# Performance work log

Hardware: AMD Instinct MI355X
Metric: run time of the kernel (lower is better)

The kernel has to match this reference:

```python
import jax, jax.numpy as jnp
import numpy as np

KERNEL_MUL = 2.0
KERNEL_NUM = 5


def setup_inputs() -> dict:
    key = jax.random.key(0)
    k1, k2 = jax.random.split(key)
    source = jax.random.normal(k1, (4096, 256), dtype=jnp.float32)
    target = jax.random.normal(k2, (4096, 256), dtype=jnp.float32)
    return {"source": source, "target": target}


def reference(source, target):
    n = source.shape[0]
    total = jnp.concatenate([source, target], axis=0)  # [2N, D]
    n_samples = total.shape[0]
    # Pairwise squared L2 distances via the norms trick (same math as
    # the broadcasted (total0 - total1)**2 sum, without the O(N^2 D) tensor).
    sq = jnp.sum(total * total, axis=-1)  # [2N]
    l2 = sq[:, None] + sq[None, :] - 2.0 * (total @ total.T)  # [2N, 2N]
    # Bandwidth is computed from .data in torch -> detached.
    bandwidth = jax.lax.stop_gradient(jnp.sum(l2)) / (n_samples ** 2 - n_samples)
    bandwidth = bandwidth / (KERNEL_MUL ** (KERNEL_NUM // 2))
    kernels = jnp.zeros_like(l2)
    for i in range(KERNEL_NUM):
        kernels = kernels + jnp.exp(-l2 / (bandwidth * KERNEL_MUL ** i))
    xx = kernels[:n, :n]
    yy = kernels[n:, n:]
    xy = kernels[:n, n:]
    yx = kernels[n:, :n]
    return jnp.mean(xx + yy - xy - yx)
```

## Files before the change

### kernel.cpp

```cpp
#include <hip/hip_runtime.h>
#include <hip/hip_bf16.h>
#if !__has_builtin(__builtin_amdgcn_cvt_pk_fp8_f32)
#include <hip/hip_fp8.h>
#endif

typedef unsigned char u8;
typedef unsigned short u16;
typedef long long i64;
typedef i64 i64x2 __attribute__((ext_vector_type(2)));
typedef float f32x4 __attribute__((ext_vector_type(4)));

#define NROW 8192
#define NHALF 4096
#define DIM 256
#define TILES 64
#define NBLK (TILES * (TILES + 1) / 2)
#define PBLK 512

static __device__ __forceinline__ float fast_exp2(float x) {
#if __has_builtin(__builtin_amdgcn_exp2f)
  return __builtin_amdgcn_exp2f(x);
#else
  return exp2f(x);
#endif
}

static __device__ __forceinline__ unsigned pack4_fp8(float4 v) {
#if __has_builtin(__builtin_amdgcn_cvt_pk_fp8_f32)
  int p = 0;
  p = __builtin_amdgcn_cvt_pk_fp8_f32(v.x, v.y, p, false);
  p = __builtin_amdgcn_cvt_pk_fp8_f32(v.z, v.w, p, true);
  return (unsigned)p;
#else
  __hip_fp8_e4m3 a(v.x), b(v.y), c(v.z), d(v.w);
  return (unsigned)a.__x | ((unsigned)b.__x << 8) | ((unsigned)c.__x << 16) |
         ((unsigned)d.__x << 24);
#endif
}


__global__ void k_prep(const float* __restrict__ src, const float* __restrict__ tgt,
                       u8* __restrict__ Xq, float* __restrict__ sq,
                       float* __restrict__ colpart) {
  __shared__ float cps[4][DIM];
  int w = threadIdx.x >> 6, lane = threadIdx.x & 63;
  int s = blockIdx.x;
  int r0 = s * 16 + w * 4;
  int p = lane >> 4, h = (lane >> 3) & 1, q = (lane >> 1) & 3, j = 4 * (lane & 1);
  float4 ca = make_float4(0.f, 0.f, 0.f, 0.f);
#pragma unroll
  for (int rr = 0; rr < 4; ++rr) {
    int row = r0 + rr;
    const float* pp = (row < NHALF) ? (src + (size_t)row * DIM)
                                    : (tgt + (size_t)(row - NHALF) * DIM);
    float4 v = *(const float4*)(pp + lane * 4);
    size_t di = ((size_t)(s * 4 + p) * 64 + q * 16 + (row & 15)) * 16 + h * 8 + j;
    *(unsigned*)(Xq + di) = pack4_fp8(v);
    ca.x += v.x; ca.y += v.y; ca.z += v.z; ca.w += v.w;
    float sum = v.x * v.x + v.y * v.y + v.z * v.z + v.w * v.w;
#pragma unroll
    for (int off = 32; off > 0; off >>= 1) sum += __shfl_down(sum, off);
    if (lane == 0) sq[row] = sum;
  }
  cps[w][lane * 4 + 0] = ca.x;
  cps[w][lane * 4 + 1] = ca.y;
  cps[w][lane * 4 + 2] = ca.z;
  cps[w][lane * 4 + 3] = ca.w;
  __syncthreads();
  int cc = threadIdx.x;
  colpart[blockIdx.x * DIM + cc] = cps[0][cc] + cps[1][cc] + cps[2][cc] + cps[3][cc];
}

__global__ void k_red(const float* __restrict__ colpart, float* __restrict__ colpart2) {
  int b = blockIdx.x, c = threadIdx.x;
  float s = 0.f;
#pragma unroll
  for (int i = 0; i < 16; ++i) s += colpart[(size_t)(b * 16 + i) * DIM + c];
  colpart2[b * DIM + c] = s;
}

__global__ void k_scal(const float* __restrict__ sq, const float* __restrict__ colpart2,
                       float* __restrict__ scal) {
  int c = threadIdx.x, lane = c & 63, w = c >> 6;
  float vs = 0.f;
#pragma unroll
  for (int b = 0; b < 32; ++b) vs += colpart2[b * DIM + c];
  float vn = vs * vs;
  float ss = 0.f;
#pragma unroll
  for (int k = 0; k < NROW / DIM; ++k) ss += sq[k * DIM + c];
#pragma unroll
  for (int off = 32; off > 0; off >>= 1) {
    vn += __shfl_down(vn, off);
    ss += __shfl_down(ss, off);
  }
  __shared__ float rv[4], rs[4];
  if (lane == 0) { rv[w] = vn; rs[w] = ss; }
  __syncthreads();
  if (c == 0) {
    double S  = (double)rs[0] + rs[1] + rs[2] + rs[3];
    double VN = (double)rv[0] + rv[1] + rv[2] + rv[3];
    double suml2 = 2.0 * (double)NROW * S - 2.0 * VN;
    double bw = suml2 / ((double)NROW * NROW - NROW) / 4.0;
    scal[0] = (float)(1.4426950408889634 / (bw * 16.0));
  }
  if (c < 32) scal[16 + c * 16] = 0.f;
}

__global__ __launch_bounds__(256, 4) void k_main(const u8* __restrict__ Xq,
                                                 const float* __restrict__ sq,
                                                 const float* __restrict__ scal,
                                                 float* __restrict__ accbuf) {
  __shared__ float red[4];

  int bi = 0, rem = blockIdx.x;
  while (rem >= TILES - bi) { rem -= TILES - bi; ++bi; }
  int bj = bi + rem;

  int tid = threadIdx.x;
  int w = tid >> 6, lane = tid & 63;
  int wi = w >> 1, wj = w & 1;

  f32x4 acc[4][4];
#pragma unroll
  for (int a = 0; a < 4; ++a)
#pragma unroll
    for (int b = 0; b < 4; ++b) acc[a][b] = (f32x4){0.f, 0.f, 0.f, 0.f};

  const i64x2* X2 = (const i64x2*)Xq;
  const int sA = bi * 8 + wi * 4;
  const int sB = bj * 8 + wj * 4;

#pragma unroll
  for (int p = 0; p < 4; ++p) {
    i64x2 aP[4], bP[4];
#pragma unroll
    for (int mi = 0; mi < 4; ++mi)
      aP[mi] = X2[(size_t)((sA + mi) * 4 + p) * 64 + lane];
#pragma unroll
    for (int ni = 0; ni < 4; ++ni)
      bP[ni] = X2[(size_t)((sB + ni) * 4 + p) * 64 + lane];
#pragma unroll
    for (int mi = 0; mi < 4; ++mi)
#pragma unroll
      for (int ni = 0; ni < 4; ++ni)
        acc[mi][ni] = __builtin_amdgcn_mfma_f32_16x16x32_fp8_fp8(
            aP[mi].x, bP[ni].x, acc[mi][ni], 0, 0, 0);
#pragma unroll
    for (int mi = 0; mi < 4; ++mi)
#pragma unroll
      for (int ni = 0; ni < 4; ++ni)
        acc[mi][ni] = __builtin_amdgcn_mfma_f32_16x16x32_fp8_fp8(
            aP[mi].y, bP[ni].y, acc[mi][ni], 0, 0, 0);
  }

  float c4 = scal[0];
  float wgt = ((bi < 32) == (bj < 32)) ? 1.f : -1.f;
  if (bi != bj) wgt *= 2.f;
  bool diag = (bi == bj);
  int ib = bi * 128 + wi * 64 + (lane >> 4) * 4;
  int jb = bj * 128 + wj * 64 + (lane & 15);
  f32x4 sqi[4];
#pragma unroll
  for (int mi = 0; mi < 4; ++mi) sqi[mi] = *(const f32x4*)(sq + ib + mi * 16);
  float lsum = 0.f;
#pragma unroll
  for (int ni = 0; ni < 4; ++ni) {
    float sqj = sq[jb + ni * 16];
#pragma unroll
    for (int mi = 0; mi < 4; ++mi) {
#pragma unroll
      for (int r = 0; r < 4; ++r) {
        float l2 = sqi[mi][r] + sqj - 2.f * acc[mi][ni][r];
        float t  = fast_exp2(-l2 * c4);
        float t2 = t * t, t4 = t2 * t2, t8 = t4 * t4, t16 = t8 * t8;
        float tt = t + t2 + t4 + t8 + t16;
        if (diag && (ib + mi * 16 + r) == (jb + ni * 16)) tt = 5.f;
        lsum += tt;
      }
    }
  }
#pragma unroll
  for (int off = 32; off > 0; off >>= 1) lsum += __shfl_down(lsum, off);
  if (lane == 0) red[w] = lsum;
  __syncthreads();
  if (tid == 0)
    atomicAdd(accbuf + (blockIdx.x & 31) * 16,
              wgt * (red[0] + red[1] + red[2] + red[3]));
}

__global__ void k_fin(const float* __restrict__ accbuf, float* __restrict__ out) {
  int lane = threadIdx.x & 63;
  float s = (lane < 32) ? accbuf[lane * 16] : 0.f;
#pragma unroll
  for (int off = 32; off > 0; off >>= 1) s += __shfl_down(s, off);
  if (threadIdx.x == 0) out[0] = s / 16777216.f;
}

extern "C" void kernel_launch(void* const* d_in, const int* in_sizes, int n_in,
                              void* d_out, int out_size, void* d_ws, size_t ws_size,
                              hipStream_t stream) {
  const float* src = (const float*)d_in[0];
  const float* tgt = (const float*)d_in[1];
  char* ws = (char*)d_ws;
  u8* Xq = (u8*)ws;
  size_t off = (size_t)NROW * DIM;
  float* sq = (float*)(ws + off);        off += NROW * 4;
  float* colpart = (float*)(ws + off);   off += (size_t)PBLK * DIM * 4;
  float* colpart2 = (float*)(ws + off);  off += (size_t)32 * DIM * 4;
  float* scal = (float*)(ws + off);
  float* out = (float*)d_out;

  k_prep<<<PBLK, 256, 0, stream>>>(src, tgt, Xq, sq, colpart);
  k_red<<<32, 256, 0, stream>>>(colpart, colpart2);
  k_scal<<<1, 256, 0, stream>>>(sq, colpart2, scal);
  k_main<<<NBLK, 256, 0, stream>>>(Xq, sq, scal, scal + 16);
  k_fin<<<1, 64, 0, stream>>>(scal + 16, out);
}
```

Measured before the change: 89.46 us.

## Stage main-kernel tiles in LDS via direct loads and fold reductions into atomics

The main kernel now copies each block's A and B fp8 tiles into LDS with global_load_lds before the MFMA loop, instead of each wave reading its fragments straight from global memory. The occupancy hint drops to 2 blocks per CU to fit the 64KB of LDS. The column-sum and squared-norm reductions become atomics in the prep kernel, which removes the k_red kernel and simplifies k_scal, at the cost of an added memset and atomic contention. Halving resident blocks could reduce latency hiding in the main kernel.

```diff
diff --git a/kernel.cpp b/kernel.cpp
--- a/kernel.cpp
+++ b/kernel.cpp
@@ -5,7 +5,6 @@
 #endif
 
 typedef unsigned char u8;
-typedef unsigned short u16;
 typedef long long i64;
 typedef i64 i64x2 __attribute__((ext_vector_type(2)));
 typedef float f32x4 __attribute__((ext_vector_type(4)));
@@ -16,6 +15,11 @@
 #define TILES 64
 #define NBLK (TILES * (TILES + 1) / 2)
 #define PBLK 512
+
+#define G_SS 256
+#define G_C4 257
+#define G_ACC 288
+#define G_ZBYTES ((G_ACC + 32 * 16) * 4)
 
 static __device__ __forceinline__ float fast_exp2(float x) {
 #if __has_builtin(__builtin_amdgcn_exp2f)
@@ -41,13 +45,14 @@
 
 __global__ void k_prep(const float* __restrict__ src, const float* __restrict__ tgt,
                        u8* __restrict__ Xq, float* __restrict__ sq,
-                       float* __restrict__ colpart) {
+                       float* __restrict__ gbuf) {
   __shared__ float cps[4][DIM];
   int w = threadIdx.x >> 6, lane = threadIdx.x & 63;
   int s = blockIdx.x;
   int r0 = s * 16 + w * 4;
   int p = lane >> 4, h = (lane >> 3) & 1, q = (lane >> 1) & 3, j = 4 * (lane & 1);
   float4 ca = make_float4(0.f, 0.f, 0.f, 0.f);
+  float ssw = 0.f;
 #pragma unroll
   for (int rr = 0; rr < 4; ++rr) {
     int row = r0 + rr;
@@ -60,57 +65,42 @@
     float sum = v.x * v.x + v.y * v.y + v.z * v.z + v.w * v.w;
 #pragma unroll
     for (int off = 32; off > 0; off >>= 1) sum += __shfl_down(sum, off);
-    if (lane == 0) sq[row] = sum;
-  }
+    if (lane == 0) { sq[row] = sum; ssw += sum; }
+  }
+  if (lane == 0) atomicAdd(gbuf + G_SS, ssw);
   cps[w][lane * 4 + 0] = ca.x;
   cps[w][lane * 4 + 1] = ca.y;
   cps[w][lane * 4 + 2] = ca.z;
   cps[w][lane * 4 + 3] = ca.w;
   __syncthreads();
   int cc = threadIdx.x;
-  colpart[blockIdx.x * DIM + cc] = cps[0][cc] + cps[1][cc] + cps[2][cc] + cps[3][cc];
-}
-
-__global__ void k_red(const float* __restrict__ colpart, float* __restrict__ colpart2) {
-  int b = blockIdx.x, c = threadIdx.x;
-  float s = 0.f;
-#pragma unroll
-  for (int i = 0; i < 16; ++i) s += colpart[(size_t)(b * 16 + i) * DIM + c];
-  colpart2[b * DIM + c] = s;
-}
-
-__global__ void k_scal(const float* __restrict__ sq, const float* __restrict__ colpart2,
-                       float* __restrict__ scal) {
+  atomicAdd(gbuf + cc, cps[0][cc] + cps[1][cc] + cps[2][cc] + cps[3][cc]);
+}
+
+__global__ void k_scal(float* __restrict__ gbuf) {
   int c = threadIdx.x, lane = c & 63, w = c >> 6;
-  float vs = 0.f;
-#pragma unroll
-  for (int b = 0; b < 32; ++b) vs += colpart2[b * DIM + c];
+  float vs = gbuf[c];
   float vn = vs * vs;
-  float ss = 0.f;
-#pragma unroll
-  for (int k = 0; k < NROW / DIM; ++k) ss += sq[k * DIM + c];
-#pragma unroll
-  for (int off = 32; off > 0; off >>= 1) {
-    vn += __shfl_down(vn, off);
-    ss += __shfl_down(ss, off);
-  }
-  __shared__ float rv[4], rs[4];
-  if (lane == 0) { rv[w] = vn; rs[w] = ss; }
+#pragma unroll
+  for (int off = 32; off > 0; off >>= 1) vn += __shfl_down(vn, off);
+  __shared__ float rv[4];
+  if (lane == 0) rv[w] = vn;
   __syncthreads();
   if (c == 0) {
-    double S  = (double)rs[0] + rs[1] + rs[2] + rs[3];
+    double S  = (double)gbuf[G_SS];
     double VN = (double)rv[0] + rv[1] + rv[2] + rv[3];
     double suml2 = 2.0 * (double)NROW * S - 2.0 * VN;
     double bw = suml2 / ((double)NROW * NROW - NROW) / 4.0;
-    scal[0] = (float)(1.4426950408889634 / (bw * 16.0));
-  }
-  if (c < 32) scal[16 + c * 16] = 0.f;
-}
-
-__global__ __launch_bounds__(256, 4) void k_main(const u8* __restrict__ Xq,
+    gbuf[G_C4] = (float)(1.4426950408889634 / (bw * 16.0));
+  }
+}
+
+__global__ __launch_bounds__(256, 2) void k_main(const u8* __restrict__ Xq,
                                                  const float* __restrict__ sq,
-                                                 const float* __restrict__ scal,
+                                                 const float* __restrict__ gbuf,
                                                  float* __restrict__ accbuf) {
+  __shared__ __align__(16) u8 Asm[32768];
+  __shared__ __align__(16) u8 Bsm[32768];
   __shared__ float red[4];
 
   int bi = 0, rem = blockIdx.x;
@@ -121,25 +111,38 @@
   int w = tid >> 6, lane = tid & 63;
   int wi = w >> 1, wj = w & 1;
 
+  const u8* Ag = Xq + (size_t)bi * 32768;
+  const u8* Bg = Xq + (size_t)bj * 32768;
+#pragma unroll
+  for (int t = 0; t < 8; ++t) {
+    int seg = t * 4 + w;
+    __builtin_amdgcn_global_load_lds(
+        (const __attribute__((address_space(1))) void*)(Ag + seg * 1024 + lane * 16),
+        (__attribute__((address_space(3))) void*)(Asm + seg * 1024), 16, 0, 0);
+    __builtin_amdgcn_global_load_lds(
+        (const __attribute__((address_space(1))) void*)(Bg + seg * 1024 + lane * 16),
+        (__attribute__((address_space(3))) void*)(Bsm + seg * 1024), 16, 0, 0);
+  }
+  __syncthreads();
+
   f32x4 acc[4][4];
 #pragma unroll
   for (int a = 0; a < 4; ++a)
 #pragma unroll
     for (int b = 0; b < 4; ++b) acc[a][b] = (f32x4){0.f, 0.f, 0.f, 0.f};
 
-  const i64x2* X2 = (const i64x2*)Xq;
-  const int sA = bi * 8 + wi * 4;
-  const int sB = bj * 8 + wj * 4;
+  const i64x2* Al = (const i64x2*)Asm;
+  const i64x2* Bl = (const i64x2*)Bsm;
 
 #pragma unroll
   for (int p = 0; p < 4; ++p) {
     i64x2 aP[4], bP[4];
 #pragma unroll
     for (int mi = 0; mi < 4; ++mi)
-      aP[mi] = X2[(size_t)((sA + mi) * 4 + p) * 64 + lane];
+      aP[mi] = Al[((wi * 4 + mi) * 4 + p) * 64 + lane];
 #pragma unroll
     for (int ni = 0; ni < 4; ++ni)
-      bP[ni] = X2[(size_t)((sB + ni) * 4 + p) * 64 + lane];
+      bP[ni] = Bl[((wj * 4 + ni) * 4 + p) * 64 + lane];
 #pragma unroll
     for (int mi = 0; mi < 4; ++mi)
 #pragma unroll
@@ -154,7 +157,7 @@
             aP[mi].y, bP[ni].y, acc[mi][ni], 0, 0, 0);
   }
 
-  float c4 = scal[0];
+  float c4 = gbuf[G_C4];
   float wgt = ((bi < 32) == (bj < 32)) ? 1.f : -1.f;
   if (bi != bj) wgt *= 2.f;
   bool diag = (bi == bj);
@@ -205,15 +208,13 @@
   char* ws = (char*)d_ws;
   u8* Xq = (u8*)ws;
   size_t off = (size_t)NROW * DIM;
-  float* sq = (float*)(ws + off);        off += NROW * 4;
-  float* colpart = (float*)(ws + off);   off += (size_t)PBLK * DIM * 4;
-  float* colpart2 = (float*)(ws + off);  off += (size_t)32 * DIM * 4;
-  float* scal = (float*)(ws + off);
+  float* sq = (float*)(ws + off);   off += NROW * 4;
+  float* gbuf = (float*)(ws + off);
   float* out = (float*)d_out;
 
-  k_prep<<<PBLK, 256, 0, stream>>>(src, tgt, Xq, sq, colpart);
-  k_red<<<32, 256, 0, stream>>>(colpart, colpart2);
-  k_scal<<<1, 256, 0, stream>>>(sq, colpart2, scal);
-  k_main<<<NBLK, 256, 0, stream>>>(Xq, sq, scal, scal + 16);
-  k_fin<<<1, 64, 0, stream>>>(scal + 16, out);
-}
+  hipMemsetAsync(gbuf, 0, G_ZBYTES, stream);
+  k_prep<<<PBLK, 256, 0, stream>>>(src, tgt, Xq, sq, gbuf);
+  k_scal<<<1, 256, 0, stream>>>(gbuf);
+  k_main<<<NBLK, 256, 0, stream>>>(Xq, sq, gbuf, gbuf + G_ACC);
+  k_fin<<<1, 64, 0, stream>>>(gbuf + G_ACC, out);
+}
```

Result: slower. 118.1 us (+32.0%).
